# Performance work log

Measured on AMD Instinct MI355X. Metric: run time of the kernel, lower is better.

The kernel has to match this reference:

```python
import jax, jax.numpy as jnp
import numpy as np

N_NODES = 100000
N_EDGES = 1250000
HIDDEN = 64


def setup_inputs() -> dict:
    key = jax.random.key(0)
    ks = jax.random.split(key, 8)
    x = jax.random.normal(ks[0], (N_NODES, HIDDEN), dtype=jnp.float32)
    edge_index = jax.random.randint(ks[1], (2, N_EDGES), 0, N_NODES, dtype=jnp.int64)
    s = 1.0 / np.sqrt(HIDDEN)
    # PyG SAGEConv params: lin_l (neighbor path, with bias), lin_r (root path, no bias)
    W1l = jax.random.uniform(ks[2], (HIDDEN, HIDDEN), jnp.float32, -s, s)
    b1l = jnp.zeros((HIDDEN,), jnp.float32)
    W1r = jax.random.uniform(ks[3], (HIDDEN, HIDDEN), jnp.float32, -s, s)
    W2l = jax.random.uniform(ks[4], (HIDDEN, HIDDEN), jnp.float32, -s, s)
    b2l = jnp.zeros((HIDDEN,), jnp.float32)
    W2r = jax.random.uniform(ks[5], (HIDDEN, HIDDEN), jnp.float32, -s, s)
    return {"x": x, "edge_index": edge_index, "W1l": W1l, "b1l": b1l,
            "W1r": W1r, "W2l": W2l, "b2l": b2l, "W2r": W2r}


def _sage_conv(x, src, dst, Wl, bl, Wr, num_nodes):
    # mean-aggregate neighbor (source) features at target nodes
    agg = jax.ops.segment_sum(x[src], dst, num_segments=num_nodes)  # [N, H]
    cnt = jax.ops.segment_sum(jnp.ones((src.shape[0],), x.dtype), dst,
                              num_segments=num_nodes)               # [N]
    mean = agg / jnp.maximum(cnt, 1.0)[:, None]
    # out = lin_l(mean_neighbors) + lin_r(x_root)
    return mean @ Wl + bl + x @ Wr


def reference(x, edge_index, W1l, b1l, W1r, W2l, b2l, W2r):
    src, dst = edge_index[0], edge_index[1]
    n = x.shape[0]
    h = jax.nn.relu(_sage_conv(x, src, dst, W1l, b1l, W1r, n))
    return _sage_conv(h, src, dst, W2l, b2l, W2r, n)
```

## Files before the change

### kernel.cpp

```cpp
#include <hip/hip_runtime.h>
#include <hip/hip_bf16.h>

#define HIDDEN 64
#define TN 64
#define APAD 132

__global__ __launch_bounds__(256) void k_hist(
    const int* __restrict__ ei, int* __restrict__ deg, int nEdges)
{
    for (int e = blockIdx.x * blockDim.x + threadIdx.x; e < nEdges;
         e += gridDim.x * blockDim.x) {
        atomicAdd(&deg[ei[nEdges + e]], 1);
    }
}

__global__ __launch_bounds__(256) void k_scan1(
    const int* __restrict__ deg, int* __restrict__ rowPtr,
    int* __restrict__ blockSum, int n)
{
    __shared__ int tmp[256];
    const int t = threadIdx.x;
    const int i = blockIdx.x * 256 + t;
    const int v = (i < n) ? deg[i] : 0;
    tmp[t] = v;
    __syncthreads();
#pragma unroll
    for (int off = 1; off < 256; off <<= 1) {
        const int u = (t >= off) ? tmp[t - off] : 0;
        __syncthreads();
        tmp[t] += u;
        __syncthreads();
    }
    if (i < n) rowPtr[i] = tmp[t] - v;
    if (t == 255) blockSum[blockIdx.x] = tmp[255];
}

__global__ __launch_bounds__(512) void k_scan2(
    int* __restrict__ blockSum, int* __restrict__ rowPtr, int nb, int n)
{
    __shared__ int tmp[512];
    const int t = threadIdx.x;
    const int v = (t < nb) ? blockSum[t] : 0;
    tmp[t] = v;
    __syncthreads();
#pragma unroll
    for (int off = 1; off < 512; off <<= 1) {
        const int u = (t >= off) ? tmp[t - off] : 0;
        __syncthreads();
        tmp[t] += u;
        __syncthreads();
    }
    if (t < nb) blockSum[t] = tmp[t] - v;
    if (t == nb - 1) rowPtr[n] = tmp[t];
}

__global__ __launch_bounds__(256) void k_scan3(
    int* __restrict__ rowPtr, int* __restrict__ cursor,
    const int* __restrict__ blockSum, int n)
{
    const int i = blockIdx.x * 256 + threadIdx.x;
    if (i < n) {
        const int v = rowPtr[i] + blockSum[blockIdx.x];
        rowPtr[i] = v;
        cursor[i] = v;
    }
}

__global__ __launch_bounds__(256) void k_fill(
    const int* __restrict__ ei, int* __restrict__ cursor,
    int* __restrict__ csrSrc, int nEdges)
{
    for (int e = blockIdx.x * blockDim.x + threadIdx.x; e < nEdges;
         e += gridDim.x * blockDim.x) {
        const int dst = ei[nEdges + e];
        const int pos = atomicAdd(&cursor[dst], 1);
        csrSrc[pos] = ei[e];
    }
}

__device__ __forceinline__ void gemm_pass(
    const float (*sA)[APAD], const float (*sB)[HIDDEN],
    int tr, int tc, int kOff, float acc[4][4])
{
#pragma unroll
    for (int k4 = 0; k4 < 16; ++k4) {
        float A_[4][4], B_[4][4];
#pragma unroll
        for (int r = 0; r < 4; ++r) {
            const float4 t4 = *(const float4*)&sA[tr * 4 + r][kOff + k4 * 4];
            A_[r][0] = t4.x; A_[r][1] = t4.y; A_[r][2] = t4.z; A_[r][3] = t4.w;
        }
#pragma unroll
        for (int kk = 0; kk < 4; ++kk) {
            const float4 t4 = *(const float4*)&sB[k4 * 4 + kk][tc * 4];
            B_[kk][0] = t4.x; B_[kk][1] = t4.y; B_[kk][2] = t4.z; B_[kk][3] = t4.w;
        }
#pragma unroll
        for (int kk = 0; kk < 4; ++kk)
#pragma unroll
            for (int r = 0; r < 4; ++r)
#pragma unroll
                for (int j = 0; j < 4; ++j)
                    acc[r][j] = fmaf(A_[r][kk], B_[kk][j], acc[r][j]);
    }
}

template <bool RELU>
__global__ __launch_bounds__(256, 3) void k_fused(
    const float* __restrict__ xin,
    const int* __restrict__ rowPtr,
    const int* __restrict__ csrSrc,
    const float* __restrict__ Wl,
    const float* __restrict__ bl,
    const float* __restrict__ Wr,
    float* __restrict__ outp,
    int nNodes)
{
    __shared__ __align__(16) float sA[TN][APAD];
    __shared__ __align__(16) float sB[HIDDEN][HIDDEN];

    const int w    = threadIdx.x >> 6;
    const int lane = threadIdx.x & 63;
    const int tr   = threadIdx.x >> 4;
    const int tc   = threadIdx.x & 15;
    const int base = blockIdx.x * TN;

    for (int i = threadIdx.x; i < HIDDEN * HIDDEN; i += 256)
        sB[i >> 6][i & 63] = Wl[i];

#pragma unroll 1
    for (int n = w * 16; n < w * 16 + 16; ++n) {
        const int g = base + n;
        float a0 = 0.f, a1 = 0.f, root = 0.f, inv = 1.f;
        if (g < nNodes) {
            const int beg = rowPtr[g], end = rowPtr[g + 1];
            if (end > beg) {
                const int last = end - 1;
#pragma unroll 1
                for (int i = beg; i < end; i += 8) {
#pragma unroll
                    for (int k = 0; k < 8; k += 2) {
                        const int iA = i + k, iB = i + k + 1;
                        const int sA_ = csrSrc[min(iA, last)];
                        const int sB_ = csrSrc[min(iB, last)];
                        const float mA = (iA < end) ? 1.f : 0.f;
                        const float mB = (iB < end) ? 1.f : 0.f;
                        a0 = fmaf(mA, xin[sA_ * HIDDEN + lane], a0);
                        a1 = fmaf(mB, xin[sB_ * HIDDEN + lane], a1);
                    }
                }
                inv = 1.0f / (float)(end - beg);
            }
            root = xin[g * HIDDEN + lane];
        }
        sA[n][lane]      = (a0 + a1) * inv;
        sA[n][64 + lane] = root;
    }
    __syncthreads();

    float acc[4][4];
#pragma unroll
    for (int r = 0; r < 4; ++r)
#pragma unroll
        for (int j = 0; j < 4; ++j) acc[r][j] = bl[tc * 4 + j];
    gemm_pass(sA, sB, tr, tc, 0, acc);

    __syncthreads();
    for (int i = threadIdx.x; i < HIDDEN * HIDDEN; i += 256)
        sB[i >> 6][i & 63] = Wr[i];
    __syncthreads();

    gemm_pass(sA, sB, tr, tc, 64, acc);

#pragma unroll
    for (int r = 0; r < 4; ++r) {
        const int g = base + tr * 4 + r;
        if (g < nNodes) {
            float4 o;
            o.x = acc[r][0]; o.y = acc[r][1]; o.z = acc[r][2]; o.w = acc[r][3];
            if (RELU) {
                o.x = fmaxf(o.x, 0.f); o.y = fmaxf(o.y, 0.f);
                o.z = fmaxf(o.z, 0.f); o.w = fmaxf(o.w, 0.f);
            }
            *(float4*)&outp[g * HIDDEN + tc * 4] = o;
        }
    }
}

extern "C" void kernel_launch(void* const* d_in, const int* in_sizes, int n_in,
                              void* d_out, int out_size, void* d_ws, size_t ws_size,
                              hipStream_t stream)
{
    const float* x   = (const float*)d_in[0];
    const int*   ei  = (const int*)d_in[1];
    const float* W1l = (const float*)d_in[2];
    const float* b1l = (const float*)d_in[3];
    const float* W1r = (const float*)d_in[4];
    const float* W2l = (const float*)d_in[5];
    const float* b2l = (const float*)d_in[6];
    const float* W2r = (const float*)d_in[7];
    float* out = (float*)d_out;

    const int nNodes = in_sizes[0] / HIDDEN;
    const int nEdges = in_sizes[1] / 2;

    float* h        = (float*)d_ws;
    int*   deg      = (int*)(h + (size_t)nNodes * HIDDEN);
    int*   rowPtr   = deg + (nNodes + 1);
    int*   cursor   = rowPtr + (nNodes + 1);
    int*   csrSrc   = cursor + nNodes;
    int*   blockSum = csrSrc + nEdges;

    const int nTiles  = (nNodes + TN - 1) / TN;
    const int nChunks = (nNodes + 255) / 256;

    hipMemsetAsync(deg, 0, (size_t)(nNodes + 1) * sizeof(int), stream);
    k_hist<<<2048, 256, 0, stream>>>(ei, deg, nEdges);
    k_scan1<<<nChunks, 256, 0, stream>>>(deg, rowPtr, blockSum, nNodes);
    k_scan2<<<1, 512, 0, stream>>>(blockSum, rowPtr, nChunks, nNodes);
    k_scan3<<<nChunks, 256, 0, stream>>>(rowPtr, cursor, blockSum, nNodes);
    k_fill<<<2048, 256, 0, stream>>>(ei, cursor, csrSrc, nEdges);

    k_fused<true><<<nTiles, 256, 0, stream>>>(x, rowPtr, csrSrc, W1l, b1l, W1r,
                                              h, nNodes);
    k_fused<false><<<nTiles, 256, 0, stream>>>(h, rowPtr, csrSrc, W2l, b2l, W2r,
                                               out, nNodes);
}
```

Before: 1.192 ms.

## Balance edge gather across tile with LDS atomics and split GEMMs into teams

Packs the destination row within its 64-node tile into the high bits of each CSR source index. Each fused block then splits the tile's whole edge range evenly across warps, accumulating gathered neighbour rows into shared memory with atomic adds instead of looping node by node, which removes load imbalance from uneven degrees. Blocks grow to 512 threads: one 256-thread team does the mean GEMM from LDS while the other does the root GEMM reading x directly from global memory, and the two results are combined through shared memory. The costs are LDS atomic contention and the packing assumption that node ids fit in 25 bits.

New measurement: 1.207 ms. About the same (+1.3%).

```diff
diff --git a/kernel.cpp b/kernel.cpp
--- a/kernel.cpp
+++ b/kernel.cpp
@@ -3,7 +3,8 @@
 
 #define HIDDEN 64
 #define TN 64
-#define APAD 132
+#define MPAD 68
+#define SRCM 0x01FFFFFF
 
 __global__ __launch_bounds__(256) void k_hist(
     const int* __restrict__ ei, int* __restrict__ deg, int nEdges)
@@ -74,39 +75,12 @@
          e += gridDim.x * blockDim.x) {
         const int dst = ei[nEdges + e];
         const int pos = atomicAdd(&cursor[dst], 1);
-        csrSrc[pos] = ei[e];
-    }
-}
-
-__device__ __forceinline__ void gemm_pass(
-    const float (*sA)[APAD], const float (*sB)[HIDDEN],
-    int tr, int tc, int kOff, float acc[4][4])
-{
-#pragma unroll
-    for (int k4 = 0; k4 < 16; ++k4) {
-        float A_[4][4], B_[4][4];
-#pragma unroll
-        for (int r = 0; r < 4; ++r) {
-            const float4 t4 = *(const float4*)&sA[tr * 4 + r][kOff + k4 * 4];
-            A_[r][0] = t4.x; A_[r][1] = t4.y; A_[r][2] = t4.z; A_[r][3] = t4.w;
-        }
-#pragma unroll
-        for (int kk = 0; kk < 4; ++kk) {
-            const float4 t4 = *(const float4*)&sB[k4 * 4 + kk][tc * 4];
-            B_[kk][0] = t4.x; B_[kk][1] = t4.y; B_[kk][2] = t4.z; B_[kk][3] = t4.w;
-        }
-#pragma unroll
-        for (int kk = 0; kk < 4; ++kk)
-#pragma unroll
-            for (int r = 0; r < 4; ++r)
-#pragma unroll
-                for (int j = 0; j < 4; ++j)
-                    acc[r][j] = fmaf(A_[r][kk], B_[kk][j], acc[r][j]);
+        csrSrc[pos] = ei[e] | ((dst & 63) << 25);
     }
 }
 
 template <bool RELU>
-__global__ __launch_bounds__(256, 3) void k_fused(
+__global__ __launch_bounds__(512, 6) void k_fused(
     const float* __restrict__ xin,
     const int* __restrict__ rowPtr,
     const int* __restrict__ csrSrc,
@@ -116,73 +90,177 @@
     float* __restrict__ outp,
     int nNodes)
 {
-    __shared__ __align__(16) float sA[TN][APAD];
-    __shared__ __align__(16) float sB[HIDDEN][HIDDEN];
-
-    const int w    = threadIdx.x >> 6;
-    const int lane = threadIdx.x & 63;
-    const int tr   = threadIdx.x >> 4;
-    const int tc   = threadIdx.x & 15;
+    __shared__ __align__(16) float sM[TN][MPAD];
+    __shared__ __align__(16) float sB[2 * HIDDEN][HIDDEN];
+    __shared__ float sInv[TN];
+
+    const int tid  = threadIdx.x;
+    const int w    = tid >> 6;
+    const int lane = tid & 63;
     const int base = blockIdx.x * TN;
 
-    for (int i = threadIdx.x; i < HIDDEN * HIDDEN; i += 256)
-        sB[i >> 6][i & 63] = Wl[i];
-
+    for (int i = tid; i < HIDDEN * HIDDEN; i += 512) {
+        sB[i >> 6][i & 63]          = Wl[i];
+        sB[(i >> 6) + HIDDEN][i & 63] = Wr[i];
+    }
+    for (int idx = tid; idx < TN * 16; idx += 512)
+        *(float4*)&sM[idx >> 4][(idx & 15) * 4] = make_float4(0.f, 0.f, 0.f, 0.f);
+    if (tid < TN) {
+        const int g = base + tid;
+        float iv = 1.f;
+        if (g < nNodes) {
+            const int d = rowPtr[g + 1] - rowPtr[g];
+            if (d > 0) iv = 1.f / (float)d;
+        }
+        sInv[tid] = iv;
+    }
+    __syncthreads();
+
+    {
+        const int eBeg = rowPtr[base];
+        const int eEnd = rowPtr[min(base + TN, nNodes)];
+        int e = eBeg + w * 8;
 #pragma unroll 1
-    for (int n = w * 16; n < w * 16 + 16; ++n) {
-        const int g = base + n;
-        float a0 = 0.f, a1 = 0.f, root = 0.f, inv = 1.f;
-        if (g < nNodes) {
-            const int beg = rowPtr[g], end = rowPtr[g + 1];
-            if (end > beg) {
-                const int last = end - 1;
+        for (; e + 8 <= eEnd; e += 64) {
+            int   pk[8];
+            float v[8];
+#pragma unroll
+            for (int k = 0; k < 8; ++k) pk[k] = csrSrc[e + k];
+#pragma unroll
+            for (int k = 0; k < 8; ++k)
+                v[k] = xin[(pk[k] & SRCM) * HIDDEN + lane];
+#pragma unroll
+            for (int k = 0; k < 8; ++k)
+                atomicAdd(&sM[pk[k] >> 25][lane], v[k]);
+        }
+        if (e < eEnd) {
 #pragma unroll 1
-                for (int i = beg; i < end; i += 8) {
-#pragma unroll
-                    for (int k = 0; k < 8; k += 2) {
-                        const int iA = i + k, iB = i + k + 1;
-                        const int sA_ = csrSrc[min(iA, last)];
-                        const int sB_ = csrSrc[min(iB, last)];
-                        const float mA = (iA < end) ? 1.f : 0.f;
-                        const float mB = (iB < end) ? 1.f : 0.f;
-                        a0 = fmaf(mA, xin[sA_ * HIDDEN + lane], a0);
-                        a1 = fmaf(mB, xin[sB_ * HIDDEN + lane], a1);
-                    }
+            for (; e < eEnd; ++e) {
+                const int p = csrSrc[e];
+                atomicAdd(&sM[p >> 25][lane], xin[(p & SRCM) * HIDDEN + lane]);
+            }
+        }
+    }
+    __syncthreads();
+
+    for (int idx = tid; idx < TN * 16; idx += 512) {
+        const int row = idx >> 4, c4 = (idx & 15) * 4;
+        float4 v = *(const float4*)&sM[row][c4];
+        const float iv = sInv[row];
+        v.x *= iv; v.y *= iv; v.z *= iv; v.w *= iv;
+        *(float4*)&sM[row][c4] = v;
+    }
+    __syncthreads();
+
+    const int team = tid >> 8;
+    const int tt   = tid & 255;
+    const int tr   = tt >> 4;
+    const int tc   = tt & 15;
+    float acc[4][4];
+
+    if (team == 0) {
+#pragma unroll
+        for (int r = 0; r < 4; ++r)
+#pragma unroll
+            for (int j = 0; j < 4; ++j) acc[r][j] = 0.f;
+#pragma unroll
+        for (int k4 = 0; k4 < 16; ++k4) {
+            float4 A4[4], B4[4];
+#pragma unroll
+            for (int r = 0; r < 4; ++r)
+                A4[r] = *(const float4*)&sM[tr * 4 + r][k4 * 4];
+#pragma unroll
+            for (int kk = 0; kk < 4; ++kk)
+                B4[kk] = *(const float4*)&sB[k4 * 4 + kk][tc * 4];
+#pragma unroll
+            for (int r = 0; r < 4; ++r) {
+                acc[r][0] = fmaf(A4[r].x, B4[0].x, acc[r][0]);
+                acc[r][1] = fmaf(A4[r].x, B4[0].y, acc[r][1]);
+                acc[r][2] = fmaf(A4[r].x, B4[0].z, acc[r][2]);
+                acc[r][3] = fmaf(A4[r].x, B4[0].w, acc[r][3]);
+                acc[r][0] = fmaf(A4[r].y, B4[1].x, acc[r][0]);
+                acc[r][1] = fmaf(A4[r].y, B4[1].y, acc[r][1]);
+                acc[r][2] = fmaf(A4[r].y, B4[1].z, acc[r][2]);
+                acc[r][3] = fmaf(A4[r].y, B4[1].w, acc[r][3]);
+                acc[r][0] = fmaf(A4[r].z, B4[2].x, acc[r][0]);
+                acc[r][1] = fmaf(A4[r].z, B4[2].y, acc[r][1]);
+                acc[r][2] = fmaf(A4[r].z, B4[2].z, acc[r][2]);
+                acc[r][3] = fmaf(A4[r].z, B4[2].w, acc[r][3]);
+                acc[r][0] = fmaf(A4[r].w, B4[3].x, acc[r][0]);
+                acc[r][1] = fmaf(A4[r].w, B4[3].y, acc[r][1]);
+                acc[r][2] = fmaf(A4[r].w, B4[3].z, acc[r][2]);
+                acc[r][3] = fmaf(A4[r].w, B4[3].w, acc[r][3]);
+            }
+        }
+    } else {
+        const float* xr[4];
+#pragma unroll
+        for (int r = 0; r < 4; ++r) {
+            int g = base + tr * 4 + r;
+            g = (g < nNodes) ? g : 0;
+            xr[r] = xin + g * HIDDEN;
+        }
+#pragma unroll
+        for (int r = 0; r < 4; ++r)
+#pragma unroll
+            for (int j = 0; j < 4; ++j) acc[r][j] = bl[tc * 4 + j];
+#pragma unroll
+        for (int k4 = 0; k4 < 16; ++k4) {
+            float4 A4[4], B4[4];
+#pragma unroll
+            for (int r = 0; r < 4; ++r)
+                A4[r] = *(const float4*)(xr[r] + k4 * 4);
+#pragma unroll
+            for (int kk = 0; kk < 4; ++kk)
+                B4[kk] = *(const float4*)&sB[HIDDEN + k4 * 4 + kk][tc * 4];
+#pragma unroll
+            for (int r = 0; r < 4; ++r) {
+                acc[r][0] = fmaf(A4[r].x, B4[0].x, acc[r][0]);
+                acc[r][1] = fmaf(A4[r].x, B4[0].y, acc[r][1]);
+                acc[r][2] = fmaf(A4[r].x, B4[0].z, acc[r][2]);
+                acc[r][3] = fmaf(A4[r].x, B4[0].w, acc[r][3]);
+                acc[r][0] = fmaf(A4[r].y, B4[1].x, acc[r][0]);
+                acc[r][1] = fmaf(A4[r].y, B4[1].y, acc[r][1]);
+                acc[r][2] = fmaf(A4[r].y, B4[1].z, acc[r][2]);
+                acc[r][3] = fmaf(A4[r].y, B4[1].w, acc[r][3]);
+                acc[r][0] = fmaf(A4[r].z, B4[2].x, acc[r][0]);
+                acc[r][1] = fmaf(A4[r].z, B4[2].y, acc[r][1]);
+                acc[r][2] = fmaf(A4[r].z, B4[2].z, acc[r][2]);
+                acc[r][3] = fmaf(A4[r].z, B4[2].w, acc[r][3]);
+                acc[r][0] = fmaf(A4[r].w, B4[3].x, acc[r][0]);
+                acc[r][1] = fmaf(A4[r].w, B4[3].y, acc[r][1]);
+                acc[r][2] = fmaf(A4[r].w, B4[3].z, acc[r][2]);
+                acc[r][3] = fmaf(A4[r].w, B4[3].w, acc[r][3]);
+            }
+        }
+    }
+    __syncthreads();
+
+    if (team == 1) {
+#pragma unroll
+        for (int r = 0; r < 4; ++r) {
+            float4 st;
+            st.x = acc[r][0]; st.y = acc[r][1];
+            st.z = acc[r][2]; st.w = acc[r][3];
+            *(float4*)&sM[tr * 4 + r][tc * 4] = st;
+        }
+    }
+    __syncthreads();
+    if (team == 0) {
+#pragma unroll
+        for (int r = 0; r < 4; ++r) {
+            const int g = base + tr * 4 + r;
+            if (g < nNodes) {
+                const float4 c4 = *(const float4*)&sM[tr * 4 + r][tc * 4];
+                float4 o;
+                o.x = acc[r][0] + c4.x; o.y = acc[r][1] + c4.y;
+                o.z = acc[r][2] + c4.z; o.w = acc[r][3] + c4.w;
+                if (RELU) {
+                    o.x = fmaxf(o.x, 0.f); o.y = fmaxf(o.y, 0.f);
+                    o.z = fmaxf(o.z, 0.f); o.w = fmaxf(o.w, 0.f);
                 }
-                inv = 1.0f / (float)(end - beg);
+                *(float4*)&outp[g * HIDDEN + tc * 4] = o;
             }
-            root = xin[g * HIDDEN + lane];
-        }
-        sA[n][lane]      = (a0 + a1) * inv;
-        sA[n][64 + lane] = root;
-    }
-    __syncthreads();
-
-    float acc[4][4];
-#pragma unroll
-    for (int r = 0; r < 4; ++r)
-#pragma unroll
-        for (int j = 0; j < 4; ++j) acc[r][j] = bl[tc * 4 + j];
-    gemm_pass(sA, sB, tr, tc, 0, acc);
-
-    __syncthreads();
-    for (int i = threadIdx.x; i < HIDDEN * HIDDEN; i += 256)
-        sB[i >> 6][i & 63] = Wr[i];
-    __syncthreads();
-
-    gemm_pass(sA, sB, tr, tc, 64, acc);
-
-#pragma unroll
-    for (int r = 0; r < 4; ++r) {
-        const int g = base + tr * 4 + r;
-        if (g < nNodes) {
-            float4 o;
-            o.x = acc[r][0]; o.y = acc[r][1]; o.z = acc[r][2]; o.w = acc[r][3];
-            if (RELU) {
-                o.x = fmaxf(o.x, 0.f); o.y = fmaxf(o.y, 0.f);
-                o.z = fmaxf(o.z, 0.f); o.w = fmaxf(o.w, 0.f);
-            }
-            *(float4*)&outp[g * HIDDEN + tc * 4] = o;
         }
     }
 }
@@ -221,8 +299,8 @@
     k_scan3<<<nChunks, 256, 0, stream>>>(rowPtr, cursor, blockSum, nNodes);
     k_fill<<<2048, 256, 0, stream>>>(ei, cursor, csrSrc, nEdges);
 
-    k_fused<true><<<nTiles, 256, 0, stream>>>(x, rowPtr, csrSrc, W1l, b1l, W1r,
+    k_fused<true><<<nTiles, 512, 0, stream>>>(x, rowPtr, csrSrc, W1l, b1l, W1r,
                                               h, nNodes);
-    k_fused<false><<<nTiles, 256, 0, stream>>>(h, rowPtr, csrSrc, W2l, b2l, W2r,
+    k_fused<false><<<nTiles, 512, 0, stream>>>(h, rowPtr, csrSrc, W2l, b2l, W2r,
                                                out, nNodes);
 }
```

## Gather bf16 features and split aggregation from the dense transform

Applied to the files above, without the earlier changes.

Converts the input features and the hidden layer to bf16 so the irregular neighbor gather moves half the bytes. Aggregation now runs in its own kernel with one wavefront per node, and the linear layers run in a separate kernel that reads bf16 mean and root rows and holds both weight matrices in shared memory. The output buffer doubles as scratch for the bf16 copy of x. In exchange the mean and root inputs lose precision relative to the fp32 reference, and each layer now writes and rereads an extra intermediate mean array.

Result: slower. 2.413 ms (+102.4%).

```diff
diff --git a/kernel.cpp b/kernel.cpp
--- a/kernel.cpp
+++ b/kernel.cpp
@@ -3,7 +3,21 @@
 
 #define HIDDEN 64
 #define TN 64
-#define APAD 132
+
+static __device__ __forceinline__ unsigned short f2bf(float f) {
+    unsigned int u = __float_as_uint(f);
+    u += 0x7FFF + ((u >> 16) & 1);
+    return (unsigned short)(u >> 16);
+}
+static __device__ __forceinline__ float bf2f(unsigned short s) {
+    return __uint_as_float((unsigned int)s << 16);
+}
+static __device__ __forceinline__ float bflo(unsigned int w) {
+    return __uint_as_float(w << 16);
+}
+static __device__ __forceinline__ float bfhi(unsigned int w) {
+    return __uint_as_float(w & 0xFFFF0000u);
+}
 
 __global__ __launch_bounds__(256) void k_hist(
     const int* __restrict__ ei, int* __restrict__ deg, int nEdges)
@@ -78,111 +92,143 @@
     }
 }
 
-__device__ __forceinline__ void gemm_pass(
-    const float (*sA)[APAD], const float (*sB)[HIDDEN],
-    int tr, int tc, int kOff, float acc[4][4])
-{
-#pragma unroll
-    for (int k4 = 0; k4 < 16; ++k4) {
-        float A_[4][4], B_[4][4];
-#pragma unroll
-        for (int r = 0; r < 4; ++r) {
-            const float4 t4 = *(const float4*)&sA[tr * 4 + r][kOff + k4 * 4];
-            A_[r][0] = t4.x; A_[r][1] = t4.y; A_[r][2] = t4.z; A_[r][3] = t4.w;
-        }
-#pragma unroll
-        for (int kk = 0; kk < 4; ++kk) {
-            const float4 t4 = *(const float4*)&sB[k4 * 4 + kk][tc * 4];
-            B_[kk][0] = t4.x; B_[kk][1] = t4.y; B_[kk][2] = t4.z; B_[kk][3] = t4.w;
-        }
-#pragma unroll
-        for (int kk = 0; kk < 4; ++kk)
-#pragma unroll
-            for (int r = 0; r < 4; ++r)
-#pragma unroll
-                for (int j = 0; j < 4; ++j)
-                    acc[r][j] = fmaf(A_[r][kk], B_[kk][j], acc[r][j]);
-    }
-}
-
-template <bool RELU>
-__global__ __launch_bounds__(256, 3) void k_fused(
-    const float* __restrict__ xin,
+__global__ __launch_bounds__(256) void k_tobf16(
+    const float* __restrict__ src, unsigned short* __restrict__ dst, int n8)
+{
+    for (int i = blockIdx.x * 256 + threadIdx.x; i < n8; i += gridDim.x * 256) {
+        const float4 a = ((const float4*)src)[2 * i];
+        const float4 b = ((const float4*)src)[2 * i + 1];
+        uint4 o;
+        o.x = (unsigned)f2bf(a.x) | ((unsigned)f2bf(a.y) << 16);
+        o.y = (unsigned)f2bf(a.z) | ((unsigned)f2bf(a.w) << 16);
+        o.z = (unsigned)f2bf(b.x) | ((unsigned)f2bf(b.y) << 16);
+        o.w = (unsigned)f2bf(b.z) | ((unsigned)f2bf(b.w) << 16);
+        ((uint4*)dst)[i] = o;
+    }
+}
+
+__global__ __launch_bounds__(256, 8) void k_agg(
+    const unsigned short* __restrict__ gtab,
     const int* __restrict__ rowPtr,
     const int* __restrict__ csrSrc,
+    unsigned short* __restrict__ meanb,
+    int nNodes)
+{
+    const int node = blockIdx.x * 4 + (threadIdx.x >> 6);
+    const int lane = threadIdx.x & 63;
+    if (node >= nNodes) return;
+    const int beg = rowPtr[node], end = rowPtr[node + 1];
+    float a0 = 0.f, a1 = 0.f;
+    int i = beg;
+#pragma unroll 1
+    for (; i + 7 < end; i += 8) {
+        const int s0 = csrSrc[i + 0], s1 = csrSrc[i + 1];
+        const int s2 = csrSrc[i + 2], s3 = csrSrc[i + 3];
+        const int s4 = csrSrc[i + 4], s5 = csrSrc[i + 5];
+        const int s6 = csrSrc[i + 6], s7 = csrSrc[i + 7];
+        a0 += bf2f(gtab[s0 * HIDDEN + lane]) + bf2f(gtab[s1 * HIDDEN + lane])
+            + bf2f(gtab[s2 * HIDDEN + lane]) + bf2f(gtab[s3 * HIDDEN + lane]);
+        a1 += bf2f(gtab[s4 * HIDDEN + lane]) + bf2f(gtab[s5 * HIDDEN + lane])
+            + bf2f(gtab[s6 * HIDDEN + lane]) + bf2f(gtab[s7 * HIDDEN + lane]);
+    }
+#pragma unroll 1
+    for (; i + 3 < end; i += 4) {
+        const int s0 = csrSrc[i + 0], s1 = csrSrc[i + 1];
+        const int s2 = csrSrc[i + 2], s3 = csrSrc[i + 3];
+        a0 += bf2f(gtab[s0 * HIDDEN + lane]) + bf2f(gtab[s1 * HIDDEN + lane]);
+        a1 += bf2f(gtab[s2 * HIDDEN + lane]) + bf2f(gtab[s3 * HIDDEN + lane]);
+    }
+#pragma unroll 1
+    for (; i < end; ++i) a0 += bf2f(gtab[csrSrc[i] * HIDDEN + lane]);
+    const float inv = (end > beg) ? 1.0f / (float)(end - beg) : 1.0f;
+    meanb[node * HIDDEN + lane] = f2bf((a0 + a1) * inv);
+}
+
+template <bool RELU, bool OUTB>
+__global__ __launch_bounds__(256, 4) void k_out(
+    const unsigned short* __restrict__ meanb,
+    const unsigned short* __restrict__ rootb,
     const float* __restrict__ Wl,
     const float* __restrict__ bl,
     const float* __restrict__ Wr,
-    float* __restrict__ outp,
+    float* __restrict__ outf,
+    unsigned short* __restrict__ outb,
     int nNodes)
 {
-    __shared__ __align__(16) float sA[TN][APAD];
-    __shared__ __align__(16) float sB[HIDDEN][HIDDEN];
-
-    const int w    = threadIdx.x >> 6;
-    const int lane = threadIdx.x & 63;
-    const int tr   = threadIdx.x >> 4;
-    const int tc   = threadIdx.x & 15;
+    __shared__ float sWl[HIDDEN][HIDDEN];
+    __shared__ float sWr[HIDDEN][HIDDEN];
+
+    const int tid = threadIdx.x;
+    for (int i = tid; i < HIDDEN * HIDDEN; i += 256) {
+        sWl[i >> 6][i & 63] = Wl[i];
+        sWr[i >> 6][i & 63] = Wr[i];
+    }
+
+    const int tr = tid >> 4;
+    const int tc = tid & 15;
     const int base = blockIdx.x * TN;
 
-    for (int i = threadIdx.x; i < HIDDEN * HIDDEN; i += 256)
-        sB[i >> 6][i & 63] = Wl[i];
-
-#pragma unroll 1
-    for (int n = w * 16; n < w * 16 + 16; ++n) {
-        const int g = base + n;
-        float a0 = 0.f, a1 = 0.f, root = 0.f, inv = 1.f;
-        if (g < nNodes) {
-            const int beg = rowPtr[g], end = rowPtr[g + 1];
-            if (end > beg) {
-                const int last = end - 1;
-#pragma unroll 1
-                for (int i = beg; i < end; i += 8) {
-#pragma unroll
-                    for (int k = 0; k < 8; k += 2) {
-                        const int iA = i + k, iB = i + k + 1;
-                        const int sA_ = csrSrc[min(iA, last)];
-                        const int sB_ = csrSrc[min(iB, last)];
-                        const float mA = (iA < end) ? 1.f : 0.f;
-                        const float mB = (iB < end) ? 1.f : 0.f;
-                        a0 = fmaf(mA, xin[sA_ * HIDDEN + lane], a0);
-                        a1 = fmaf(mB, xin[sB_ * HIDDEN + lane], a1);
-                    }
-                }
-                inv = 1.0f / (float)(end - beg);
+    const float b0 = bl[tc * 4 + 0], b1 = bl[tc * 4 + 1];
+    const float b2 = bl[tc * 4 + 2], b3 = bl[tc * 4 + 3];
+
+    float acc[4][4];
+#pragma unroll
+    for (int r = 0; r < 4; ++r) {
+        acc[r][0] = b0; acc[r][1] = b1; acc[r][2] = b2; acc[r][3] = b3;
+    }
+    int gr[4];
+#pragma unroll
+    for (int r = 0; r < 4; ++r) {
+        const int g = base + tr * 4 + r;
+        gr[r] = (g < nNodes) ? g : (nNodes - 1);
+    }
+    __syncthreads();
+
+#pragma unroll
+    for (int k8 = 0; k8 < 8; ++k8) {
+        unsigned int am[4][4], ar[4][4];
+#pragma unroll
+        for (int r = 0; r < 4; ++r) {
+            const uint4 m4 = *(const uint4*)&meanb[gr[r] * HIDDEN + k8 * 8];
+            const uint4 r4 = *(const uint4*)&rootb[gr[r] * HIDDEN + k8 * 8];
+            am[r][0] = m4.x; am[r][1] = m4.y; am[r][2] = m4.z; am[r][3] = m4.w;
+            ar[r][0] = r4.x; ar[r][1] = r4.y; ar[r][2] = r4.z; ar[r][3] = r4.w;
+        }
+#pragma unroll
+        for (int kk = 0; kk < 8; ++kk) {
+            const float4 wl4 = *(const float4*)&sWl[k8 * 8 + kk][tc * 4];
+            const float4 wr4 = *(const float4*)&sWr[k8 * 8 + kk][tc * 4];
+#pragma unroll
+            for (int r = 0; r < 4; ++r) {
+                const unsigned int wm = am[r][kk >> 1];
+                const unsigned int wq = ar[r][kk >> 1];
+                const float aM = (kk & 1) ? bfhi(wm) : bflo(wm);
+                const float aR = (kk & 1) ? bfhi(wq) : bflo(wq);
+                acc[r][0] = fmaf(aM, wl4.x, fmaf(aR, wr4.x, acc[r][0]));
+                acc[r][1] = fmaf(aM, wl4.y, fmaf(aR, wr4.y, acc[r][1]));
+                acc[r][2] = fmaf(aM, wl4.z, fmaf(aR, wr4.z, acc[r][2]));
+                acc[r][3] = fmaf(aM, wl4.w, fmaf(aR, wr4.w, acc[r][3]));
             }
-            root = xin[g * HIDDEN + lane];
         }
-        sA[n][lane]      = (a0 + a1) * inv;
-        sA[n][64 + lane] = root;
-    }
-    __syncthreads();
-
-    float acc[4][4];
-#pragma unroll
-    for (int r = 0; r < 4; ++r)
-#pragma unroll
-        for (int j = 0; j < 4; ++j) acc[r][j] = bl[tc * 4 + j];
-    gemm_pass(sA, sB, tr, tc, 0, acc);
-
-    __syncthreads();
-    for (int i = threadIdx.x; i < HIDDEN * HIDDEN; i += 256)
-        sB[i >> 6][i & 63] = Wr[i];
-    __syncthreads();
-
-    gemm_pass(sA, sB, tr, tc, 64, acc);
+    }
 
 #pragma unroll
     for (int r = 0; r < 4; ++r) {
         const int g = base + tr * 4 + r;
         if (g < nNodes) {
-            float4 o;
-            o.x = acc[r][0]; o.y = acc[r][1]; o.z = acc[r][2]; o.w = acc[r][3];
+            float o0 = acc[r][0], o1 = acc[r][1], o2 = acc[r][2], o3 = acc[r][3];
             if (RELU) {
-                o.x = fmaxf(o.x, 0.f); o.y = fmaxf(o.y, 0.f);
-                o.z = fmaxf(o.z, 0.f); o.w = fmaxf(o.w, 0.f);
+                o0 = fmaxf(o0, 0.f); o1 = fmaxf(o1, 0.f);
+                o2 = fmaxf(o2, 0.f); o3 = fmaxf(o3, 0.f);
             }
-            *(float4*)&outp[g * HIDDEN + tc * 4] = o;
+            if (OUTB) {
+                ushort4 q;
+                q.x = f2bf(o0); q.y = f2bf(o1); q.z = f2bf(o2); q.w = f2bf(o3);
+                *(ushort4*)&outb[g * HIDDEN + tc * 4] = q;
+            } else {
+                float4 o; o.x = o0; o.y = o1; o.z = o2; o.w = o3;
+                *(float4*)&outf[g * HIDDEN + tc * 4] = o;
+            }
         }
     }
 }
@@ -204,15 +250,19 @@
     const int nNodes = in_sizes[0] / HIDDEN;
     const int nEdges = in_sizes[1] / 2;
 
-    float* h        = (float*)d_ws;
-    int*   deg      = (int*)(h + (size_t)nNodes * HIDDEN);
-    int*   rowPtr   = deg + (nNodes + 1);
-    int*   cursor   = rowPtr + (nNodes + 1);
-    int*   csrSrc   = cursor + nNodes;
-    int*   blockSum = csrSrc + nEdges;
+    unsigned short* meanb    = (unsigned short*)d_ws;
+    unsigned short* cb2      = meanb + (size_t)nNodes * HIDDEN;
+    int*            deg      = (int*)(cb2 + (size_t)nNodes * HIDDEN);
+    int*            rowPtr   = deg + (nNodes + 1);
+    int*            cursor   = rowPtr + (nNodes + 1);
+    int*            csrSrc   = cursor + nNodes;
+    int*            blockSum = csrSrc + nEdges;
+    unsigned short* cb1      = (unsigned short*)d_out;
 
     const int nTiles  = (nNodes + TN - 1) / TN;
     const int nChunks = (nNodes + 255) / 256;
+    const int nFeat8  = nNodes * HIDDEN / 8;
+    const int aggGrid = (nNodes + 3) / 4;
 
     hipMemsetAsync(deg, 0, (size_t)(nNodes + 1) * sizeof(int), stream);
     k_hist<<<2048, 256, 0, stream>>>(ei, deg, nEdges);
@@ -221,8 +271,12 @@
     k_scan3<<<nChunks, 256, 0, stream>>>(rowPtr, cursor, blockSum, nNodes);
     k_fill<<<2048, 256, 0, stream>>>(ei, cursor, csrSrc, nEdges);
 
-    k_fused<true><<<nTiles, 256, 0, stream>>>(x, rowPtr, csrSrc, W1l, b1l, W1r,
-                                              h, nNodes);
-    k_fused<false><<<nTiles, 256, 0, stream>>>(h, rowPtr, csrSrc, W2l, b2l, W2r,
-                                               out, nNodes);
-}
+    k_tobf16<<<2048, 256, 0, stream>>>(x, cb1, nFeat8);
+    k_agg<<<aggGrid, 256, 0, stream>>>(cb1, rowPtr, csrSrc, meanb, nNodes);
+    k_out<true, true><<<nTiles, 256, 0, stream>>>(
+        meanb, cb1, W1l, b1l, W1r, nullptr, cb2, nNodes);
+
+    k_agg<<<aggGrid, 256, 0, stream>>>(cb2, rowPtr, csrSrc, meanb, nNodes);
+    k_out<false, false><<<nTiles, 256, 0, stream>>>(
+        meanb, cb2, W2l, b2l, W2r, out, nullptr, nNodes);
+}
```
